# Performance work log

Measured on AMD Instinct MI355X. Metric: run time of the kernel, lower is better.

The kernel has to match this reference:

```python
import jax, jax.numpy as jnp
import numpy as np

B, T, D = 4, 2048, 1024
H = 16
HD = D // H  # 64

def setup_inputs() -> dict:
    key = jax.random.key(0)
    ks = jax.random.split(key, 7)
    s = 1.0 / np.sqrt(D)
    x = jax.random.normal(ks[0], (B, T, D), dtype=jnp.float32)
    # Per-head query projections stacked: Wq[h] maps D -> HD
    Wq = jax.random.uniform(ks[1], (H, D, HD), minval=-s, maxval=s, dtype=jnp.float32)
    bq = jax.random.uniform(ks[2], (H, HD), minval=-s, maxval=s, dtype=jnp.float32)
    Wk = jax.random.uniform(ks[3], (D, HD), minval=-s, maxval=s, dtype=jnp.float32)
    bk = jax.random.uniform(ks[4], (HD,), minval=-s, maxval=s, dtype=jnp.float32)
    Wv = jax.random.uniform(ks[5], (D, HD), minval=-s, maxval=s, dtype=jnp.float32)
    bv = jax.random.uniform(ks[6], (HD,), minval=-s, maxval=s, dtype=jnp.float32)
    return {"x": x, "Wq": Wq, "bq": bq, "Wk": Wk, "bk": bk, "Wv": Wv, "bv": bv}

def reference(x, Wq, bq, Wk, bk, Wv, bv):
    # shared single K/V head: [B, T, HD]
    k = jnp.einsum('btd,de->bte', x, Wk) + bk
    v = jnp.einsum('btd,de->bte', x, Wv) + bv
    # per-head queries batched: [B, H, T, HD]
    q = jnp.einsum('btd,hde->bhte', x, Wq) + bq[:, None, :]
    scale = 1.0 / jnp.sqrt(jnp.asarray(HD, dtype=x.dtype))
    scores = jnp.einsum('bhqe,bke->bhqk', q, k) * scale  # [B, H, T, T]
    attn = jax.nn.softmax(scores, axis=-1)
    out = jnp.einsum('bhqk,bke->bhqe', attn, v)  # [B, H, T, HD]
    # concat heads along last dim (head order matches torch cat order)
    return jnp.transpose(out, (0, 2, 1, 3)).reshape(B, T, H * HD)
```

## Files before the change

### kernel.cpp

```cpp
#include <hip/hip_runtime.h>

#define B 4
#define T 2048
#define D 1024
#define H 16
#define HD 64
#define NKT 32

typedef __attribute__((ext_vector_type(8))) short bf16x8;
typedef __attribute__((ext_vector_type(4))) float f32x4;
typedef __attribute__((ext_vector_type(16))) float f32x16;

#define MFMA16(a, b, c) __builtin_amdgcn_mfma_f32_16x16x32_bf16(a, b, c, 0, 0, 0)
#define MFMA32(a, b, c) __builtin_amdgcn_mfma_f32_32x32x16_bf16(a, b, c, 0, 0, 0)

static __device__ __forceinline__ unsigned short f2bf(float f) {
    union { float f; unsigned u; } v; v.f = f;
    unsigned r = v.u + 0x7FFFu + ((v.u >> 16) & 1u);
    return (unsigned short)(r >> 16);
}

static __device__ __forceinline__ bf16x8 cvt8(const float* p) {
    float4 a = *(const float4*)p;
    float4 b = *(const float4*)(p + 4);
    bf16x8 r;
    r[0] = (short)f2bf(a.x); r[1] = (short)f2bf(a.y);
    r[2] = (short)f2bf(a.z); r[3] = (short)f2bf(a.w);
    r[4] = (short)f2bf(b.x); r[5] = (short)f2bf(b.y);
    r[6] = (short)f2bf(b.z); r[7] = (short)f2bf(b.w);
    return r;
}

static __device__ __forceinline__ unsigned cvtpk(float lo, float hi) {
    unsigned r;
    asm("v_cvt_pk_bf16_f32 %0, %1, %2" : "=v"(r) : "v"(lo), "v"(hi));
    return r;
}

static __device__ __forceinline__ float fmax3(float a, float b, float c) {
    return fmaxf(fmaxf(a, b), c);
}

static __device__ __forceinline__ f32x16 zero16() {
    f32x16 z;
#pragma unroll
    for (int i = 0; i < 16; ++i) z[i] = 0.f;
    return z;
}

static __device__ __forceinline__ float xhalf_max(float x) {
    unsigned u = __float_as_uint(x);
    auto r = __builtin_amdgcn_permlane32_swap(u, u, false, false);
    return fmaxf(__uint_as_float(r[0]), __uint_as_float(r[1]));
}
static __device__ __forceinline__ float xhalf_sum(float x) {
    unsigned u = __float_as_uint(x);
    auto r = __builtin_amdgcn_permlane32_swap(u, u, false, false);
    return __uint_as_float(r[0]) + __uint_as_float(r[1]);
}

typedef __attribute__((address_space(1))) const unsigned char gl_u8;
typedef __attribute__((address_space(3))) unsigned char lds_u8;

static __device__ __forceinline__ void stage16(const void* g, void* l) {
    __builtin_amdgcn_global_load_lds((gl_u8*)(unsigned long long)g,
                                     (lds_u8*)(unsigned int)(unsigned long long)l,
                                     16, 0, 0);
}

__global__ __launch_bounds__(256) void pack_w(const float* __restrict__ Wq,
                                              const float* __restrict__ Wk,
                                              const float* __restrict__ Wv,
                                              unsigned short* __restrict__ Wqt,
                                              unsigned short* __restrict__ Wkt,
                                              unsigned short* __restrict__ Wvt) {
    __shared__ float tile[64][65];
    int hh = blockIdx.x >> 4, db = blockIdx.x & 15;
    const float* src;
    unsigned short* dst;
    if (hh < 16)      { src = Wq + (size_t)hh * D * HD; dst = Wqt + (size_t)hh * HD * D; }
    else if (hh == 16){ src = Wk; dst = Wkt; }
    else              { src = Wv; dst = Wvt; }
    int r = threadIdx.x >> 6, c = threadIdx.x & 63;
    int d0 = db * 64;
#pragma unroll
    for (int i = 0; i < 16; ++i)
        tile[r * 16 + i][c] = src[(size_t)(d0 + r * 16 + i) * HD + c];
    __syncthreads();
#pragma unroll
    for (int j = 0; j < 16; ++j)
        dst[(size_t)(r * 16 + j) * D + d0 + c] = f2bf(tile[c][r * 16 + j]);
}

__global__ __launch_bounds__(256) void kv_gemm(const float* __restrict__ xf,
                                               const unsigned short* __restrict__ Wkt,
                                               const unsigned short* __restrict__ Wvt,
                                               const float* __restrict__ bk,
                                               const float* __restrict__ bv,
                                               unsigned short* __restrict__ xbf,
                                               unsigned char* __restrict__ Ksw,
                                               unsigned char* __restrict__ Vsw) {
    int grp = blockIdx.x >> 7;
    int rtb = blockIdx.x & 127;
    int wave = threadIdx.x >> 6;
    int lane = threadIdx.x & 63;
    int ln = lane & 15, lk = lane >> 4;
    int rt = rtb * 4 + wave;
    int t0 = rt * 16;

    const unsigned short* Wt = grp ? Wvt : Wkt;
    const float* bias = grp ? bv : bk;

    f32x4 acc[4];
#pragma unroll
    for (int e = 0; e < 4; ++e) acc[e] = (f32x4){0.f, 0.f, 0.f, 0.f};

    for (int d0 = 0; d0 < D; d0 += 32) {
        size_t xi = (size_t)(t0 + ln) * D + d0 + lk * 8;
        bf16x8 a = cvt8(xf + xi);
        if (grp == 0) *(bf16x8*)(xbf + xi) = a;
#pragma unroll
        for (int e = 0; e < 4; ++e) {
            bf16x8 w = *(const bf16x8*)(Wt + (size_t)(e * 16 + ln) * D + d0 + lk * 8);
            acc[e] = MFMA16(a, w, acc[e]);
        }
    }

#pragma unroll
    for (int e = 0; e < 4; ++e)
#pragma unroll
        for (int r = 0; r < 4; ++r) {
            int trow = t0 + lk * 4 + r;
            float val = acc[e][r] + bias[e * 16 + ln];
            int bb = trow >> 11, tl = trow & 2047;
            size_t tbase = ((size_t)(bb * NKT + (tl >> 6))) << 13;
            int key = tl & 63;
            if (grp == 0) {
                int off = (e * 2 + (key >> 5)) * 1024 +
                          ((ln >> 3) * 32 + (key & 31)) * 16 + (ln & 7) * 2;
                *(unsigned short*)(Ksw + tbase + off) = f2bf(val);
            } else {
                int off = ((key >> 4) * 2 + (e >> 1)) * 1024 +
                          (((key >> 3) & 1) * 32 + (e & 1) * 16 + ln) * 16 +
                          (key & 7) * 2;
                *(unsigned short*)(Vsw + tbase + off) = f2bf(val);
            }
        }
}

__global__ __launch_bounds__(256, 4) void attn(const unsigned short* __restrict__ xbf,
                                               const unsigned short* __restrict__ Wqt,
                                               const float* __restrict__ bq,
                                               const unsigned char* __restrict__ Ksw,
                                               const unsigned char* __restrict__ Vsw,
                                               float* __restrict__ out) {
    __shared__ __align__(16) unsigned char smem[32768];

    int blk = ((blockIdx.x & 7) << 7) | (blockIdx.x >> 3);
    int qt = blk & 15;
    int h  = (blk >> 4) & 15;
    int b  = blk >> 8;
    int wave = threadIdx.x >> 6, lane = threadIdx.x & 63;
    int l31 = lane & 31, hi = lane >> 5;
    int t0 = qt * 128 + wave * 32;

    const unsigned char* Kt = Ksw + (((size_t)b * NKT) << 13);
    const unsigned char* Vt = Vsw + (((size_t)b * NKT) << 13);
    int soff = wave * 1024 + lane * 16;
    int ldsw = wave * 1024;

    auto STAGE = [&](int kt, int lk, int lv) {
        const unsigned char* gK = Kt + ((size_t)kt << 13);
        const unsigned char* gV = Vt + ((size_t)kt << 13);
        stage16(gK + soff,        smem + lk + ldsw);
        stage16(gK + 4096 + soff, smem + lk + 4096 + ldsw);
        stage16(gV + soff,        smem + lv + ldsw);
        stage16(gV + 4096 + soff, smem + lv + 4096 + ldsw);
    };

    STAGE(0, 0, 16384);

    f32x16 qacc[2] = {zero16(), zero16()};
    const unsigned short* Wh = Wqt + (size_t)h * HD * D;
    const unsigned short* xrow  = xbf + (size_t)(b * T + t0 + l31) * D + hi * 8;
    const unsigned short* wrow0 = Wh + (size_t)l31 * D + hi * 8;
    const unsigned short* wrow1 = Wh + (size_t)(32 + l31) * D + hi * 8;
    for (int dk = 0; dk < D; dk += 16) {
        bf16x8 xb = *(const bf16x8*)(xrow + dk);
        qacc[0] = MFMA32(*(const bf16x8*)(wrow0 + dk), xb, qacc[0]);
        qacc[1] = MFMA32(*(const bf16x8*)(wrow1 + dk), xb, qacc[1]);
    }

    const float sl2 = 0.125f * 1.44269504f;
    float qv[2][16];
#pragma unroll
    for (int e0 = 0; e0 < 2; ++e0)
#pragma unroll
        for (int r = 0; r < 16; ++r) {
            int crow = (r & 3) + 8 * (r >> 2) + 4 * hi;
            qv[e0][r] = (qacc[e0][r] + bq[h * HD + e0 * 32 + crow]) * sl2;
        }

    bf16x8 qf[4];
#pragma unroll
    for (int dt = 0; dt < 4; ++dt) {
        int s = dt >> 1;
        int b0 = 8 * (dt & 1), b1 = b0 + 4;
        unsigned c0 = cvtpk(qv[s][b0 + 0], qv[s][b0 + 1]);
        unsigned c1 = cvtpk(qv[s][b0 + 2], qv[s][b0 + 3]);
        unsigned c2 = cvtpk(qv[s][b1 + 0], qv[s][b1 + 1]);
        unsigned c3 = cvtpk(qv[s][b1 + 2], qv[s][b1 + 3]);
        auto r02 = __builtin_amdgcn_permlane32_swap(c0, c2, false, false);
        auto r13 = __builtin_amdgcn_permlane32_swap(c1, c3, false, false);
        union { unsigned u[4]; bf16x8 v; } pu;
        pu.u[0] = r02[0]; pu.u[1] = r13[0]; pu.u[2] = r02[1]; pu.u[3] = r13[1];
        qf[dt] = pu.v;
    }

    const unsigned char* fbase = smem + lane * 16;

    __syncthreads();

    float mrun = -1e30f, lrun = 0.f;
    f32x16 o[2] = {zero16(), zero16()};

    auto TILE = [&](int ck, int cv, int nxt, int nk, int nv) {
        if (nxt < NKT) STAGE(nxt, nk, nv);

        f32x16 sacc[2] = {zero16(), zero16()};
        __builtin_amdgcn_s_setprio(1);
#pragma unroll
        for (int dt = 0; dt < 4; ++dt) {
            bf16x8 kf0 = *(const bf16x8*)(fbase + ck + (dt * 2 + 0) * 1024);
            bf16x8 kf1 = *(const bf16x8*)(fbase + ck + (dt * 2 + 1) * 1024);
            sacc[0] = MFMA32(kf0, qf[dt], sacc[0]);
            sacc[1] = MFMA32(kf1, qf[dt], sacc[1]);
        }
        __builtin_amdgcn_s_setprio(0);

#define SV(j) (sacc[(j) >> 4][(j) & 15])
        float mt[11];
#pragma unroll
        for (int i = 0; i < 10; ++i)
            mt[i] = fmax3(SV(3 * i), SV(3 * i + 1), SV(3 * i + 2));
        mt[10] = fmaxf(SV(30), SV(31));
        float y0 = fmax3(mt[0], mt[1], mt[2]);
        float y1 = fmax3(mt[3], mt[4], mt[5]);
        float y2 = fmax3(mt[6], mt[7], mt[8]);
        float y3 = fmax3(mt[9], mt[10], y0);
        float pmax = xhalf_max(fmax3(y1, y2, y3));
#undef SV

        if (__any(pmax - mrun > 8.0f)) {
            float newm = fmaxf(mrun, pmax);
            float corr = __builtin_amdgcn_exp2f(mrun - newm);
            mrun = newm;
            lrun *= corr;
#pragma unroll
            for (int e0 = 0; e0 < 2; ++e0)
#pragma unroll
                for (int r = 0; r < 16; ++r) o[e0][r] *= corr;
        }

#pragma unroll
        for (int kt2 = 0; kt2 < 2; ++kt2)
#pragma unroll
            for (int r = 0; r < 16; ++r)
                sacc[kt2][r] = __builtin_amdgcn_exp2f(sacc[kt2][r] - mrun);

        float sm[8];
#pragma unroll
        for (int i = 0; i < 8; ++i)
            sm[i] = (sacc[0][i] + sacc[0][i + 8]) + (sacc[1][i] + sacc[1][i + 8]);
#pragma unroll
        for (int i = 0; i < 4; ++i) sm[i] += sm[i + 4];
        float rsum = (sm[0] + sm[1]) + (sm[2] + sm[3]);
        lrun += xhalf_sum(rsum);

        __builtin_amdgcn_s_setprio(1);
#pragma unroll
        for (int ks = 0; ks < 4; ++ks) {
            int s = ks >> 1;
            int b0 = 8 * (ks & 1), b1 = b0 + 4;
            bf16x8 vf0 = *(const bf16x8*)(fbase + cv + (ks * 2 + 0) * 1024);
            bf16x8 vf1 = *(const bf16x8*)(fbase + cv + (ks * 2 + 1) * 1024);
            unsigned c0 = cvtpk(sacc[s][b0 + 0], sacc[s][b0 + 1]);
            unsigned c1 = cvtpk(sacc[s][b0 + 2], sacc[s][b0 + 3]);
            unsigned c2 = cvtpk(sacc[s][b1 + 0], sacc[s][b1 + 1]);
            unsigned c3 = cvtpk(sacc[s][b1 + 2], sacc[s][b1 + 3]);
            auto r02 = __builtin_amdgcn_permlane32_swap(c0, c2, false, false);
            auto r13 = __builtin_amdgcn_permlane32_swap(c1, c3, false, false);
            union { unsigned u[4]; bf16x8 v; } pu;
            pu.u[0] = r02[0]; pu.u[1] = r13[0]; pu.u[2] = r02[1]; pu.u[3] = r13[1];
            o[0] = MFMA32(vf0, pu.v, o[0]);
            o[1] = MFMA32(vf1, pu.v, o[1]);
        }
        __builtin_amdgcn_s_setprio(0);

        __syncthreads();
    };

    for (int kt = 0; kt < NKT; kt += 2) {
        TILE(0,    16384, kt + 1, 8192, 24576);
        TILE(8192, 24576, kt + 2, 0,    16384);
    }

    float inv = 1.f / lrun;
    unsigned char* eb = smem + wave * 8192;
#pragma unroll
    for (int e0 = 0; e0 < 2; ++e0)
#pragma unroll
        for (int r = 0; r < 16; ++r) {
            int crow = (r & 3) + 8 * (r >> 2) + 4 * hi;
            int col4 = (e0 * 32 + crow) * 4;
            *(float*)(eb + l31 * 256 + (col4 ^ ((l31 & 15) << 4))) = o[e0][r] * inv;
        }
    __syncthreads();

    int rgrp = lane >> 4;
    int c16 = (lane & 15) * 16;
#pragma unroll
    for (int g = 0; g < 8; ++g) {
        int row = g * 4 + rgrp;
        float4 vv = *(const float4*)(eb + row * 256 + (c16 ^ ((row & 15) << 4)));
        *(float4*)(out + (size_t)(b * T + t0 + row) * D + h * HD + (c16 >> 2)) = vv;
    }
}

extern "C" void kernel_launch(void* const* d_in, const int* in_sizes, int n_in,
                              void* d_out, int out_size, void* d_ws, size_t ws_size,
                              hipStream_t stream) {
    const float* x  = (const float*)d_in[0];
    const float* Wq = (const float*)d_in[1];
    const float* bq = (const float*)d_in[2];
    const float* Wk = (const float*)d_in[3];
    const float* bk = (const float*)d_in[4];
    const float* Wv = (const float*)d_in[5];
    const float* bv = (const float*)d_in[6];
    float* out = (float*)d_out;

    unsigned char* ws = (unsigned char*)d_ws;
    unsigned short* xbf = (unsigned short*)(ws);
    unsigned short* Wqt = (unsigned short*)(ws + 16777216);
    unsigned short* Wkt = (unsigned short*)(ws + 18874368);
    unsigned short* Wvt = (unsigned short*)(ws + 19005440);
    unsigned char*  Ksw = ws + 19136512;
    unsigned char*  Vsw = ws + 20185088;

    pack_w<<<288, 256, 0, stream>>>(Wq, Wk, Wv, Wqt, Wkt, Wvt);
    kv_gemm<<<256, 256, 0, stream>>>(x, Wkt, Wvt, bk, bv, xbf, Ksw, Vsw);
    attn<<<1024, 256, 0, stream>>>(xbf, Wqt, bq, Ksw, Vsw, out);
}
```

Measured before the change: 181.2 us.

## Software-pipeline QK of the next tile with softmax and PV of the current

Splits K and V staging into separate lambdas and reorders the attention loop. The QK^T MFMAs for tile i+1 are now issued before the softmax and PV for tile i, using two sets of score accumulators and staggered K and V buffers. The aim is to overlap the exp and reduction VALU work with matrix-core work and to start loads earlier. The cost is 32 extra live accumulator registers per lane, which may lower occupancy or cause spills, and the buffer reuse now depends on the barrier placement being exactly right.

Result: slower. 207.7 us (+14.6%).

```diff
diff --git a/kernel.cpp b/kernel.cpp
--- a/kernel.cpp
+++ b/kernel.cpp
@@ -169,16 +169,20 @@
     int soff = wave * 1024 + lane * 16;
     int ldsw = wave * 1024;
 
-    auto STAGE = [&](int kt, int lk, int lv) {
-        const unsigned char* gK = Kt + ((size_t)kt << 13);
-        const unsigned char* gV = Vt + ((size_t)kt << 13);
-        stage16(gK + soff,        smem + lk + ldsw);
-        stage16(gK + 4096 + soff, smem + lk + 4096 + ldsw);
-        stage16(gV + soff,        smem + lv + ldsw);
-        stage16(gV + 4096 + soff, smem + lv + 4096 + ldsw);
+    auto STAGEK = [&](int kt, int lb) {
+        const unsigned char* g = Kt + ((size_t)kt << 13);
+        stage16(g + soff,        smem + lb + ldsw);
+        stage16(g + 4096 + soff, smem + lb + 4096 + ldsw);
     };
-
-    STAGE(0, 0, 16384);
+    auto STAGEV = [&](int kt, int lb) {
+        const unsigned char* g = Vt + ((size_t)kt << 13);
+        stage16(g + soff,        smem + lb + ldsw);
+        stage16(g + 4096 + soff, smem + lb + 4096 + ldsw);
+    };
+
+    STAGEK(0, 0);
+    STAGEV(0, 16384);
+    STAGEK(1, 8192);
 
     f32x16 qacc[2] = {zero16(), zero16()};
     const unsigned short* Wh = Wqt + (size_t)h * HD * D;
@@ -219,37 +223,34 @@
 
     const unsigned char* fbase = smem + lane * 16;
 
-    __syncthreads();
-
     float mrun = -1e30f, lrun = 0.f;
     f32x16 o[2] = {zero16(), zero16()};
-
-    auto TILE = [&](int ck, int cv, int nxt, int nk, int nv) {
-        if (nxt < NKT) STAGE(nxt, nk, nv);
-
-        f32x16 sacc[2] = {zero16(), zero16()};
-        __builtin_amdgcn_s_setprio(1);
+    f32x16 sA0, sA1, sB0, sB1;
+
+    auto QK = [&](f32x16& s0, f32x16& s1, int ck) {
+        s0 = zero16(); s1 = zero16();
 #pragma unroll
         for (int dt = 0; dt < 4; ++dt) {
             bf16x8 kf0 = *(const bf16x8*)(fbase + ck + (dt * 2 + 0) * 1024);
             bf16x8 kf1 = *(const bf16x8*)(fbase + ck + (dt * 2 + 1) * 1024);
-            sacc[0] = MFMA32(kf0, qf[dt], sacc[0]);
-            sacc[1] = MFMA32(kf1, qf[dt], sacc[1]);
-        }
-        __builtin_amdgcn_s_setprio(0);
-
-#define SV(j) (sacc[(j) >> 4][(j) & 15])
+            s0 = MFMA32(kf0, qf[dt], s0);
+            s1 = MFMA32(kf1, qf[dt], s1);
+        }
+    };
+
+    auto SMPV = [&](f32x16& s0, f32x16& s1, int cv) {
+#define SV(j) ((j) < 16 ? s0[(j) & 15] : s1[(j) & 15])
         float mt[11];
 #pragma unroll
         for (int i = 0; i < 10; ++i)
             mt[i] = fmax3(SV(3 * i), SV(3 * i + 1), SV(3 * i + 2));
         mt[10] = fmaxf(SV(30), SV(31));
+#undef SV
         float y0 = fmax3(mt[0], mt[1], mt[2]);
         float y1 = fmax3(mt[3], mt[4], mt[5]);
         float y2 = fmax3(mt[6], mt[7], mt[8]);
         float y3 = fmax3(mt[9], mt[10], y0);
         float pmax = xhalf_max(fmax3(y1, y2, y3));
-#undef SV
 
         if (__any(pmax - mrun > 8.0f)) {
             float newm = fmaxf(mrun, pmax);
@@ -263,46 +264,60 @@
         }
 
 #pragma unroll
-        for (int kt2 = 0; kt2 < 2; ++kt2)
-#pragma unroll
-            for (int r = 0; r < 16; ++r)
-                sacc[kt2][r] = __builtin_amdgcn_exp2f(sacc[kt2][r] - mrun);
+        for (int r = 0; r < 16; ++r) {
+            s0[r] = __builtin_amdgcn_exp2f(s0[r] - mrun);
+            s1[r] = __builtin_amdgcn_exp2f(s1[r] - mrun);
+        }
 
         float sm[8];
 #pragma unroll
         for (int i = 0; i < 8; ++i)
-            sm[i] = (sacc[0][i] + sacc[0][i + 8]) + (sacc[1][i] + sacc[1][i + 8]);
+            sm[i] = (s0[i] + s0[i + 8]) + (s1[i] + s1[i + 8]);
 #pragma unroll
         for (int i = 0; i < 4; ++i) sm[i] += sm[i + 4];
         float rsum = (sm[0] + sm[1]) + (sm[2] + sm[3]);
         lrun += xhalf_sum(rsum);
 
         __builtin_amdgcn_s_setprio(1);
-#pragma unroll
-        for (int ks = 0; ks < 4; ++ks) {
-            int s = ks >> 1;
-            int b0 = 8 * (ks & 1), b1 = b0 + 4;
-            bf16x8 vf0 = *(const bf16x8*)(fbase + cv + (ks * 2 + 0) * 1024);
-            bf16x8 vf1 = *(const bf16x8*)(fbase + cv + (ks * 2 + 1) * 1024);
-            unsigned c0 = cvtpk(sacc[s][b0 + 0], sacc[s][b0 + 1]);
-            unsigned c1 = cvtpk(sacc[s][b0 + 2], sacc[s][b0 + 3]);
-            unsigned c2 = cvtpk(sacc[s][b1 + 0], sacc[s][b1 + 1]);
-            unsigned c3 = cvtpk(sacc[s][b1 + 2], sacc[s][b1 + 3]);
-            auto r02 = __builtin_amdgcn_permlane32_swap(c0, c2, false, false);
-            auto r13 = __builtin_amdgcn_permlane32_swap(c1, c3, false, false);
-            union { unsigned u[4]; bf16x8 v; } pu;
-            pu.u[0] = r02[0]; pu.u[1] = r13[0]; pu.u[2] = r02[1]; pu.u[3] = r13[1];
-            o[0] = MFMA32(vf0, pu.v, o[0]);
-            o[1] = MFMA32(vf1, pu.v, o[1]);
-        }
+#define PVKS(SS, ks)                                                          \
+        {                                                                     \
+            const int b0 = 8 * ((ks) & 1), b1 = b0 + 4;                       \
+            bf16x8 vf0 = *(const bf16x8*)(fbase + cv + ((ks) * 2 + 0) * 1024);\
+            bf16x8 vf1 = *(const bf16x8*)(fbase + cv + ((ks) * 2 + 1) * 1024);\
+            unsigned c0 = cvtpk(SS[b0 + 0], SS[b0 + 1]);                      \
+            unsigned c1 = cvtpk(SS[b0 + 2], SS[b0 + 3]);                      \
+            unsigned c2 = cvtpk(SS[b1 + 0], SS[b1 + 1]);                      \
+            unsigned c3 = cvtpk(SS[b1 + 2], SS[b1 + 3]);                      \
+            auto r02 = __builtin_amdgcn_permlane32_swap(c0, c2, false, false);\
+            auto r13 = __builtin_amdgcn_permlane32_swap(c1, c3, false, false);\
+            union { unsigned u[4]; bf16x8 v; } pu;                            \
+            pu.u[0] = r02[0]; pu.u[1] = r13[0];                               \
+            pu.u[2] = r02[1]; pu.u[3] = r13[1];                               \
+            o[0] = MFMA32(vf0, pu.v, o[0]);                                   \
+            o[1] = MFMA32(vf1, pu.v, o[1]);                                   \
+        }
+        PVKS(s0, 0); PVKS(s0, 1); PVKS(s1, 2); PVKS(s1, 3);
+#undef PVKS
         __builtin_amdgcn_s_setprio(0);
-
+    };
+
+    __syncthreads();
+    QK(sA0, sA1, 0);
+    __syncthreads();
+
+    for (int i = 0; i < NKT; i += 2) {
+        if (i + 2 < NKT) STAGEK(i + 2, 0);
+        STAGEV(i + 1, 24576);
+        QK(sB0, sB1, 8192);
+        SMPV(sA0, sA1, 16384);
         __syncthreads();
-    };
-
-    for (int kt = 0; kt < NKT; kt += 2) {
-        TILE(0,    16384, kt + 1, 8192, 24576);
-        TILE(8192, 24576, kt + 2, 0,    16384);
+        if (i + 3 < NKT) STAGEK(i + 3, 8192);
+        if (i + 2 < NKT) {
+            STAGEV(i + 2, 16384);
+            QK(sA0, sA1, 0);
+        }
+        SMPV(sB0, sB1, 24576);
+        __syncthreads();
     }
 
     float inv = 1.f / lrun;
```

## Split attention tile into two 32-key phases and interleave K/V waves in kv_gemm

Applied to the files above, without the earlier changes.

The attention inner tile now processes its 64 keys as two sequential 32-key phases, each with its own score accumulator, max update, exp and PV MFMA. This halves live score registers, which may raise occupancy or cut spills, but it adds an extra max/rescale check per tile and shortens the MFMA chains available for overlap. The setprio hints are removed. Separately, kv_gemm now puts K and V waves for the same row tiles in one block instead of splitting them across block groups, so both share the same x rows within a block.

Result: no change. 183.0 us (+1.0%).

```diff
diff --git a/kernel.cpp b/kernel.cpp
--- a/kernel.cpp
+++ b/kernel.cpp
@@ -100,12 +100,10 @@
                                                unsigned short* __restrict__ xbf,
                                                unsigned char* __restrict__ Ksw,
                                                unsigned char* __restrict__ Vsw) {
-    int grp = blockIdx.x >> 7;
-    int rtb = blockIdx.x & 127;
-    int wave = threadIdx.x >> 6;
+    int rt  = blockIdx.x * 2 + (threadIdx.x >> 7);
+    int grp = (threadIdx.x >> 6) & 1;
     int lane = threadIdx.x & 63;
     int ln = lane & 15, lk = lane >> 4;
-    int rt = rtb * 4 + wave;
     int t0 = rt * 16;
 
     const unsigned short* Wt = grp ? Wvt : Wkt;
@@ -224,32 +222,22 @@
     float mrun = -1e30f, lrun = 0.f;
     f32x16 o[2] = {zero16(), zero16()};
 
-    auto TILE = [&](int ck, int cv, int nxt, int nk, int nv) {
-        if (nxt < NKT) STAGE(nxt, nk, nv);
-
-        f32x16 sacc[2] = {zero16(), zero16()};
-        __builtin_amdgcn_s_setprio(1);
+    auto PHASE = [&](int ck, int cv, int ph) {
+        f32x16 s = zero16();
 #pragma unroll
         for (int dt = 0; dt < 4; ++dt) {
-            bf16x8 kf0 = *(const bf16x8*)(fbase + ck + (dt * 2 + 0) * 1024);
-            bf16x8 kf1 = *(const bf16x8*)(fbase + ck + (dt * 2 + 1) * 1024);
-            sacc[0] = MFMA32(kf0, qf[dt], sacc[0]);
-            sacc[1] = MFMA32(kf1, qf[dt], sacc[1]);
-        }
-        __builtin_amdgcn_s_setprio(0);
-
-#define SV(j) (sacc[(j) >> 4][(j) & 15])
-        float mt[11];
-#pragma unroll
-        for (int i = 0; i < 10; ++i)
-            mt[i] = fmax3(SV(3 * i), SV(3 * i + 1), SV(3 * i + 2));
-        mt[10] = fmaxf(SV(30), SV(31));
-        float y0 = fmax3(mt[0], mt[1], mt[2]);
-        float y1 = fmax3(mt[3], mt[4], mt[5]);
-        float y2 = fmax3(mt[6], mt[7], mt[8]);
-        float y3 = fmax3(mt[9], mt[10], y0);
-        float pmax = xhalf_max(fmax3(y1, y2, y3));
-#undef SV
+            bf16x8 kf = *(const bf16x8*)(fbase + ck + (dt * 2 + ph) * 1024);
+            s = MFMA32(kf, qf[dt], s);
+        }
+
+        float m0 = fmax3(s[0], s[1], s[2]);
+        float m1 = fmax3(s[3], s[4], s[5]);
+        float m2 = fmax3(s[6], s[7], s[8]);
+        float m3 = fmax3(s[9], s[10], s[11]);
+        float m4 = fmax3(s[12], s[13], s[14]);
+        float y0 = fmax3(m0, m1, m2);
+        float y1 = fmax3(m3, m4, s[15]);
+        float pmax = xhalf_max(fmaxf(y0, y1));
 
         if (__any(pmax - mrun > 8.0f)) {
             float newm = fmaxf(mrun, pmax);
@@ -263,31 +251,26 @@
         }
 
 #pragma unroll
-        for (int kt2 = 0; kt2 < 2; ++kt2)
-#pragma unroll
-            for (int r = 0; r < 16; ++r)
-                sacc[kt2][r] = __builtin_amdgcn_exp2f(sacc[kt2][r] - mrun);
+        for (int r = 0; r < 16; ++r)
+            s[r] = __builtin_amdgcn_exp2f(s[r] - mrun);
 
         float sm[8];
 #pragma unroll
-        for (int i = 0; i < 8; ++i)
-            sm[i] = (sacc[0][i] + sacc[0][i + 8]) + (sacc[1][i] + sacc[1][i + 8]);
+        for (int i = 0; i < 8; ++i) sm[i] = s[i] + s[i + 8];
 #pragma unroll
         for (int i = 0; i < 4; ++i) sm[i] += sm[i + 4];
         float rsum = (sm[0] + sm[1]) + (sm[2] + sm[3]);
         lrun += xhalf_sum(rsum);
 
-        __builtin_amdgcn_s_setprio(1);
-#pragma unroll
-        for (int ks = 0; ks < 4; ++ks) {
-            int s = ks >> 1;
-            int b0 = 8 * (ks & 1), b1 = b0 + 4;
-            bf16x8 vf0 = *(const bf16x8*)(fbase + cv + (ks * 2 + 0) * 1024);
-            bf16x8 vf1 = *(const bf16x8*)(fbase + cv + (ks * 2 + 1) * 1024);
-            unsigned c0 = cvtpk(sacc[s][b0 + 0], sacc[s][b0 + 1]);
-            unsigned c1 = cvtpk(sacc[s][b0 + 2], sacc[s][b0 + 3]);
-            unsigned c2 = cvtpk(sacc[s][b1 + 0], sacc[s][b1 + 1]);
-            unsigned c3 = cvtpk(sacc[s][b1 + 2], sacc[s][b1 + 3]);
+#pragma unroll
+        for (int ks = 0; ks < 2; ++ks) {
+            int b0 = 8 * ks, b1 = b0 + 4;
+            bf16x8 vf0 = *(const bf16x8*)(fbase + cv + ((ph * 2 + ks) * 2 + 0) * 1024);
+            bf16x8 vf1 = *(const bf16x8*)(fbase + cv + ((ph * 2 + ks) * 2 + 1) * 1024);
+            unsigned c0 = cvtpk(s[b0 + 0], s[b0 + 1]);
+            unsigned c1 = cvtpk(s[b0 + 2], s[b0 + 3]);
+            unsigned c2 = cvtpk(s[b1 + 0], s[b1 + 1]);
+            unsigned c3 = cvtpk(s[b1 + 2], s[b1 + 3]);
             auto r02 = __builtin_amdgcn_permlane32_swap(c0, c2, false, false);
             auto r13 = __builtin_amdgcn_permlane32_swap(c1, c3, false, false);
             union { unsigned u[4]; bf16x8 v; } pu;
@@ -295,8 +278,12 @@
             o[0] = MFMA32(vf0, pu.v, o[0]);
             o[1] = MFMA32(vf1, pu.v, o[1]);
         }
-        __builtin_amdgcn_s_setprio(0);
-
+    };
+
+    auto TILE = [&](int ck, int cv, int nxt, int nk, int nv) {
+        if (nxt < NKT) STAGE(nxt, nk, nv);
+        PHASE(ck, cv, 0);
+        PHASE(ck, cv, 1);
         __syncthreads();
     };
 
```
